# Kernel optimization log

Hardware: AMD Instinct MI355X
Metric: run time of the kernel (lower is better)

Reference implementation:

```python
import jax, jax.numpy as jnp
import numpy as np


def setup_inputs() -> dict:
    key = jax.random.key(0)
    ks = jax.random.split(key, 6)
    B, H, W, C = 4, 56, 56, 256
    NH, K = 8, 7
    return {
        "x": jax.random.normal(ks[0], (B, H, W, C), dtype=jnp.float32),
        "w_qkv": jax.random.normal(ks[1], (C, 3 * C), dtype=jnp.float32) * 0.02,
        "b_qkv": jax.random.normal(ks[2], (3 * C,), dtype=jnp.float32) * 0.02,
        "rpb": jax.random.normal(ks[3], (NH, K * K), dtype=jnp.float32) * 0.02,
        "w_proj": jax.random.normal(ks[4], (C, C), dtype=jnp.float32) * 0.02,
        "b_proj": jax.random.normal(ks[5], (C,), dtype=jnp.float32) * 0.02,
    }


def _window_stack(xp, H, W, ks):
    # xp: (B, H+2p, W+2p, nh, hd) zero-padded map.
    # Returns (B, H, W, nh, ks*ks, hd): each pixel's ks x ks neighborhood,
    # row-major (h offset outer, w offset inner) to match torch unfold order.
    return jnp.stack(
        [xp[:, i:i + H, j:j + W] for i in range(ks) for j in range(ks)],
        axis=-2,
    )


def reference(x, w_qkv, b_qkv, rpb, w_proj, b_proj):
    B, H, W, C = x.shape
    nh, ks2 = rpb.shape
    ks = int(np.sqrt(ks2) + 0.5)  # 7
    hd = C // nh
    scale = hd ** -0.5
    pad = ks // 2  # dilation == 1

    qkv = (x @ w_qkv + b_qkv).reshape(B, H, W, 3, nh, hd)
    q = qkv[..., 0, :, :] * scale        # (B,H,W,nh,hd)
    k = qkv[..., 1, :, :]
    v = qkv[..., 2, :, :]

    pads = ((0, 0), (pad, pad), (pad, pad), (0, 0), (0, 0))
    kw = _window_stack(jnp.pad(k, pads), H, W, ks)  # (B,H,W,nh,ks2,hd)
    vw = _window_stack(jnp.pad(v, pads), H, W, ks)

    # scores over each pixel's ks*ks neighbors (zero-padded borders kept,
    # matching the torch reference), plus relative position bias.
    attn = jnp.einsum("bhwnd,bhwnkd->bhwnk", q, kw) + rpb[None, None, None]
    attn = jax.nn.softmax(attn, axis=-1)
    out = jnp.einsum("bhwnk,bhwnkd->bhwnd", attn, vw).reshape(B, H, W, C)
    return out @ w_proj + b_proj
```

## Files before the change

kernel.cpp:

```cpp
#include <hip/hip_runtime.h>
#include <hip/hip_bf16.h>


using frag_ab = __attribute__((ext_vector_type(8))) short;
using f32x4   = __attribute__((ext_vector_type(4))) float;
using f32x2   = __attribute__((ext_vector_type(2))) float;

typedef const __attribute__((address_space(1))) unsigned int* gas_u32;
typedef __attribute__((address_space(3))) unsigned int*       las_u32;

__device__ __forceinline__ void gl_lds16(const void* g, void* l) {
    __builtin_amdgcn_global_load_lds((gas_u32)g, (las_u32)l, 16, 0, 0);
}

__device__ __forceinline__ float bflo(unsigned int u) { return __uint_as_float(u << 16); }
__device__ __forceinline__ float bfhi(unsigned int u) { return __uint_as_float(u & 0xffff0000u); }

__device__ __forceinline__ f32x2 unpk2(unsigned int u) {
    f32x2 r; r.x = bflo(u); r.y = bfhi(u); return r;
}

#if defined(__has_builtin)
#if __has_builtin(__builtin_amdgcn_fdot2_f32_bf16)
#define HAVE_FDOT2_BF16 1
#endif
#endif

#ifdef HAVE_FDOT2_BF16
typedef __bf16 bf16x2 __attribute__((ext_vector_type(2)));
__device__ __forceinline__ float dot2bf(unsigned int a, unsigned int b, float c) {
    union { unsigned int u; bf16x2 h; } ua, ub;
    ua.u = a; ub.u = b;
    return __builtin_amdgcn_fdot2_f32_bf16(ua.h, ub.h, c, false);
}
#endif

__global__ __launch_bounds__(256) void prep_k(
    const float* __restrict__ w_qkv,  __hip_bfloat16* __restrict__ wqkvT,
    const float* __restrict__ w_proj, __hip_bfloat16* __restrict__ wprojT,
    __hip_bfloat16* __restrict__ kp,  __hip_bfloat16* __restrict__ vp)
{
    const int bid = blockIdx.x;
    const int tid = threadIdx.x;
    if (bid < 768) {
        const int idx = bid * 256 + tid;
        const int k = idx & 255, n = idx >> 8;
        wqkvT[idx] = __float2bfloat16(w_qkv[k * 768 + n]);
    } else if (bid < 1024) {
        const int idx = (bid - 768) * 256 + tid;
        const int k = idx & 255, n = idx >> 8;
        wprojT[idx] = __float2bfloat16(w_proj[k * 256 + n]);
    } else {
        const int u    = (bid - 1024) * 256 + tid;
        const int ip   = u / 30720;
        const int rem  = u - ip * 30720;
        const int cloc = rem >> 5;
        const int q16  = rem & 31;
        const int img  = ip >> 1;
        __hip_bfloat16* base = (ip & 1) ? vp : kp;
        int prow, pcol;
        if (cloc < 512) {
            const int r8 = cloc >> 6;
            prow = (r8 < 3) ? r8 : r8 + 56;
            pcol = cloc & 63;
        } else {
            const int c2 = cloc - 512;
            prow = 3 + (c2 >> 3);
            const int cc = c2 & 7;
            pcol = (cc < 3) ? cc : cc + 56;
        }
        *(uint4*)(base + (((size_t)(img * 64 + prow)) * 64 + pcol) * 256 + q16 * 8) =
            make_uint4(0u, 0u, 0u, 0u);
    }
}

__global__ __launch_bounds__(256) void gemm_qkv_k(
    const float* __restrict__ X,
    const __hip_bfloat16* __restrict__ BT,
    const float* __restrict__ bias,
    __hip_bfloat16* __restrict__ qf,
    __hip_bfloat16* __restrict__ kp,
    __hip_bfloat16* __restrict__ vp,
    float qscale)
{
    constexpr int K = 256;
    __shared__ float   Asf[8][2][64][4];
    __shared__ frag_ab Bs[8][64];

    const int tid  = threadIdx.x;
    const int lane = tid & 63;
    const int w    = tid >> 6;
    const int wm   = w >> 1, wn = w & 1;
    const int m0 = blockIdx.y * 128;
    const int n0 = blockIdx.x * 128;

    const int lrow = lane & 15;
    const int lk   = (lane >> 4) * 8;
    const float* gA0 = X + (size_t)(m0 + (2*w+0)*16 + lrow) * K + lk;
    const float* gA1 = X + (size_t)(m0 + (2*w+1)*16 + lrow) * K + lk;
    const __hip_bfloat16* gB0 = BT + (size_t)(n0 + (2*w+0)*16 + lrow) * K + lk;
    const __hip_bfloat16* gB1 = BT + (size_t)(n0 + (2*w+1)*16 + lrow) * K + lk;

    f32x4 acc[4][4] = {};

    for (int k0 = 0; k0 < K; k0 += 32) {
        gl_lds16(gA0 + k0,     &Asf[2*w+0][0][0][0]);
        gl_lds16(gA0 + k0 + 4, &Asf[2*w+0][1][0][0]);
        gl_lds16(gA1 + k0,     &Asf[2*w+1][0][0][0]);
        gl_lds16(gA1 + k0 + 4, &Asf[2*w+1][1][0][0]);
        gl_lds16(gB0 + k0, &Bs[2*w+0][0]);
        gl_lds16(gB1 + k0, &Bs[2*w+1][0]);
        __syncthreads();
        frag_ab af[4], bf[4];
        #pragma unroll
        for (int i = 0; i < 4; ++i) {
            const float4 c0 = *(const float4*)&Asf[wm*4+i][0][lane][0];
            const float4 c1 = *(const float4*)&Asf[wm*4+i][1][lane][0];
            union { frag_ab f; __hip_bfloat16 h[8]; } u;
            u.h[0] = __float2bfloat16(c0.x); u.h[1] = __float2bfloat16(c0.y);
            u.h[2] = __float2bfloat16(c0.z); u.h[3] = __float2bfloat16(c0.w);
            u.h[4] = __float2bfloat16(c1.x); u.h[5] = __float2bfloat16(c1.y);
            u.h[6] = __float2bfloat16(c1.z); u.h[7] = __float2bfloat16(c1.w);
            af[i] = u.f;
            bf[i] = Bs[wn*4+i][lane];
        }
        #pragma unroll
        for (int i = 0; i < 4; ++i)
            #pragma unroll
            for (int j = 0; j < 4; ++j)
                acc[i][j] = __builtin_amdgcn_mfma_f32_16x16x32_bf16(af[i], bf[j], acc[i][j], 0, 0, 0);
        __syncthreads();
    }

    const int rbase = (lane >> 4) * 4;
    const int cbase = lane & 15;
    #pragma unroll
    for (int fi = 0; fi < 4; ++fi) {
        const int rm = m0 + wm * 64 + fi * 16 + rbase;
        #pragma unroll
        for (int fj = 0; fj < 4; ++fj) {
            const int cn = n0 + wn * 64 + fj * 16 + cbase;
            const float bv = bias[cn];
            #pragma unroll
            for (int r = 0; r < 4; ++r) {
                const int mm  = rm + r;
                const float val = acc[fi][fj][r] + bv;
                const int sel = cn >> 8;
                if (sel == 0) {
                    qf[(size_t)mm * 256 + cn] = __float2bfloat16(val * qscale);
                } else {
                    const int c  = cn & 255;
                    const int bb = mm / 3136;
                    const int r2 = mm % 3136;
                    const int yy = r2 / 56;
                    const int xx = r2 % 56;
                    __hip_bfloat16* dst = (sel == 1) ? kp : vp;
                    dst[(((size_t)(bb * 64 + yy + 3)) * 64 + (xx + 3)) * 256 + c] =
                        __float2bfloat16(val);
                }
            }
        }
    }
}

__global__ __launch_bounds__(256) void gemm_proj_k(
    const __hip_bfloat16* __restrict__ A,
    const __hip_bfloat16* __restrict__ BT,
    const float* __restrict__ bias,
    float* __restrict__ C)
{
    constexpr int K = 256;
    __shared__ frag_ab As[4][64];
    __shared__ frag_ab Bs[4][64];

    const int tid  = threadIdx.x;
    const int lane = tid & 63;
    const int w    = tid >> 6;
    const int wm   = w >> 1, wn = w & 1;
    const int m0 = blockIdx.y * 64;
    const int n0 = blockIdx.x * 64;

    const int lrow = lane & 15;
    const int lk   = (lane >> 4) * 8;
    const __hip_bfloat16* gA = A  + (size_t)(m0 + w * 16 + lrow) * K + lk;
    const __hip_bfloat16* gB = BT + (size_t)(n0 + w * 16 + lrow) * K + lk;

    f32x4 acc[2][2] = {};

    for (int k0 = 0; k0 < K; k0 += 32) {
        gl_lds16(gA + k0, &As[w][0]);
        gl_lds16(gB + k0, &Bs[w][0]);
        __syncthreads();
        const frag_ab a0 = As[2 * wm + 0][lane];
        const frag_ab a1 = As[2 * wm + 1][lane];
        const frag_ab b0 = Bs[2 * wn + 0][lane];
        const frag_ab b1 = Bs[2 * wn + 1][lane];
        acc[0][0] = __builtin_amdgcn_mfma_f32_16x16x32_bf16(a0, b0, acc[0][0], 0, 0, 0);
        acc[0][1] = __builtin_amdgcn_mfma_f32_16x16x32_bf16(a0, b1, acc[0][1], 0, 0, 0);
        acc[1][0] = __builtin_amdgcn_mfma_f32_16x16x32_bf16(a1, b0, acc[1][0], 0, 0, 0);
        acc[1][1] = __builtin_amdgcn_mfma_f32_16x16x32_bf16(a1, b1, acc[1][1], 0, 0, 0);
        __syncthreads();
    }

    const int rbase = (lane >> 4) * 4;
    const int cbase = lane & 15;
    #pragma unroll
    for (int fi = 0; fi < 2; ++fi) {
        const int rm = m0 + wm * 32 + fi * 16 + rbase;
        #pragma unroll
        for (int fj = 0; fj < 2; ++fj) {
            const int cn = n0 + wn * 32 + fj * 16 + cbase;
            const float bv = bias[cn];
            #pragma unroll
            for (int r = 0; r < 4; ++r)
                C[(size_t)(rm + r) * 256 + cn] = acc[fi][fj][r] + bv;
        }
    }
}

__global__ __launch_bounds__(64) void na2d_attn_k(
    const __hip_bfloat16* __restrict__ qf,
    const __hip_bfloat16* __restrict__ kp,
    const __hip_bfloat16* __restrict__ vp,
    const float* __restrict__ rpb,
    __hip_bfloat16* __restrict__ out)
{
    const int lane = threadIdx.x;
    const int q8   = lane & 3;
    const int h    = (lane >> 2) & 7;
    const int tl   = (lane >> 5) & 1;

    const int bid = blockIdx.x;
    const int seg = (bid & 7) * 784 + (bid >> 3);
    const int row = seg / 28;
    const int x0  = (seg % 28) * 2;
    const int b   = row / 56;
    const int y   = row % 56;
    const int t   = row * 56 + x0 + tl;
    const int prow0 = b * 64 + y;

    __shared__ __hip_bfloat16 kbuf[8 * 256];
    __shared__ float srpb[8 * 49];

    for (int i = lane; i < 8 * 49; i += 64) srpb[i] = rpb[i];
    __syncthreads();

    unsigned int qpk[4];
    {
        const uint4 qa = *(const uint4*)(qf + (size_t)t * 256 + h * 32 + q8 * 8);
        qpk[0] = qa.x; qpk[1] = qa.y; qpk[2] = qa.z; qpk[3] = qa.w;
    }
#ifndef HAVE_FDOT2_BF16
    f32x2 q2[4];
    #pragma unroll
    for (int i = 0; i < 4; ++i) q2[i] = unpk2(qpk[i]);
#endif

    const int wroff = lane * 16;
    const int rdoff = tl * 512 + h * 64 + q8 * 16;

#define GLOAD4(plane, ky, d0, d1, d2, d3)                                       \
    do {                                                                        \
        const char* rb_ = (const char*)((plane) +                               \
            ((size_t)(prow0 + (ky)) * 64 + x0) * 256 + lane * 8);               \
        d0 = *(const uint4*)(rb_);                                              \
        d1 = *(const uint4*)(rb_ + 1024);                                       \
        d2 = *(const uint4*)(rb_ + 2048);                                       \
        d3 = *(const uint4*)(rb_ + 3072);                                       \
    } while (0)

#define LWRITE4(buf, s0, s1, s2, s3)                                            \
    do {                                                                        \
        char* wb_ = (char*)(buf) + wroff;                                       \
        *(uint4*)(wb_)        = s0;                                             \
        *(uint4*)(wb_ + 1024) = s1;                                             \
        *(uint4*)(wb_ + 2048) = s2;                                             \
        *(uint4*)(wb_ + 3072) = s3;                                             \
    } while (0)

    const float* rp = &srpb[h * 49];
    float m = -1e30f, l = 0.f;
    f32x2 o2[4] = {};

    uint4 k0, k1, k2, k3;
    GLOAD4(kp, 0, k0, k1, k2, k3);

    #pragma unroll 1
    for (int ky = 0; ky < 7; ++ky) {
        LWRITE4(kbuf, k0, k1, k2, k3);
        const __hip_bfloat16* vrow = vp +
            ((size_t)(prow0 + ky) * 64 + x0 + tl) * 256 + h * 32 + q8 * 8;
        uint4 va[7];
        #pragma unroll
        for (int kx = 0; kx < 7; ++kx)
            va[kx] = *(const uint4*)(vrow + kx * 256);
        if (ky < 6) GLOAD4(kp, ky + 1, k0, k1, k2, k3);
        float lg[7];
        #pragma unroll
        for (int kx = 0; kx < 7; ++kx) {
            const uint4 w0 = *(const uint4*)((const char*)kbuf + rdoff + kx * 512);
#ifdef HAVE_FDOT2_BF16
            float s = 0.f;
            s = dot2bf(qpk[0], w0.x, s);
            s = dot2bf(qpk[1], w0.y, s);
            s = dot2bf(qpk[2], w0.z, s);
            s = dot2bf(qpk[3], w0.w, s);
#else
            f32x2 s2 = {0.f, 0.f};
            s2 += q2[0] * unpk2(w0.x);
            s2 += q2[1] * unpk2(w0.y);
            s2 += q2[2] * unpk2(w0.z);
            s2 += q2[3] * unpk2(w0.w);
            const float s = s2.x + s2.y;
#endif
            lg[kx] = s;
        }
        #pragma unroll
        for (int kx = 0; kx < 7; ++kx) {
            lg[kx] += __shfl_xor(lg[kx], 1, 64);
            lg[kx] += __shfl_xor(lg[kx], 2, 64);
            lg[kx] += rp[ky * 7 + kx];
        }
        float rmax = lg[0];
        #pragma unroll
        for (int kx = 1; kx < 7; ++kx) rmax = fmaxf(rmax, lg[kx]);
        const float mnew  = fmaxf(m, rmax);
        const float alpha = __expf(m - mnew);
        m = mnew;
        l *= alpha;
        const f32x2 alpha2 = {alpha, alpha};
        #pragma unroll
        for (int i = 0; i < 4; ++i) o2[i] *= alpha2;
        #pragma unroll
        for (int kx = 0; kx < 7; ++kx) {
            const float pr = __expf(lg[kx] - mnew);
            l += pr;
            const f32x2 pr2 = {pr, pr};
            const uint4 w0 = va[kx];
            o2[0] += pr2 * unpk2(w0.x);
            o2[1] += pr2 * unpk2(w0.y);
            o2[2] += pr2 * unpk2(w0.z);
            o2[3] += pr2 * unpk2(w0.w);
        }
    }
#undef GLOAD4
#undef LWRITE4

    const float inv = 1.f / l;
    union { uint4 u; __hip_bfloat16 hh[8]; } ob;
    #pragma unroll
    for (int i = 0; i < 4; ++i) {
        ob.hh[2 * i + 0] = __float2bfloat16(o2[i].x * inv);
        ob.hh[2 * i + 1] = __float2bfloat16(o2[i].y * inv);
    }
    *(uint4*)(out + (size_t)t * 256 + h * 32 + q8 * 8) = ob.u;
}

extern "C" void kernel_launch(void* const* d_in, const int* in_sizes, int n_in,
                              void* d_out, int out_size, void* d_ws, size_t ws_size,
                              hipStream_t stream)
{
    const float* x      = (const float*)d_in[0];
    const float* w_qkv  = (const float*)d_in[1];
    const float* b_qkv  = (const float*)d_in[2];
    const float* rpb    = (const float*)d_in[3];
    const float* w_proj = (const float*)d_in[4];
    const float* b_proj = (const float*)d_in[5];
    float* out = (float*)d_out;

    const int M = 12544;

    char* wsp = (char*)d_ws;
    __hip_bfloat16* qf    = (__hip_bfloat16*)wsp; wsp += (size_t)M * 256 * 2;
    __hip_bfloat16* kp    = (__hip_bfloat16*)wsp; wsp += (size_t)4 * 64 * 64 * 256 * 2;
    __hip_bfloat16* vp    = (__hip_bfloat16*)wsp; wsp += (size_t)4 * 64 * 64 * 256 * 2;
    __hip_bfloat16* attnb = (__hip_bfloat16*)wsp; wsp += (size_t)M * 256 * 2;
    __hip_bfloat16* wqkvT = (__hip_bfloat16*)wsp; wsp += (size_t)768 * 256 * 2;
    __hip_bfloat16* wprojT= (__hip_bfloat16*)wsp; wsp += (size_t)256 * 256 * 2;

    const float scale = 0.17677669529663689f;

    prep_k<<<1984, 256, 0, stream>>>(w_qkv, wqkvT, w_proj, wprojT, kp, vp);

    gemm_qkv_k<<<dim3(6, 98), 256, 0, stream>>>(x, wqkvT, b_qkv, qf, kp, vp, scale);

    na2d_attn_k<<<6272, 64, 0, stream>>>(qf, kp, vp, rpb, attnb);

    gemm_proj_k<<<dim3(4, 196), 256, 0, stream>>>(attnb, wprojT, b_proj, out);
}
```

Measured before the change: 137.9 us.

## Pre-convert x to bf16 and double-buffer LDS tiles in both GEMMs

The prep kernel gains a pass that converts the fp32 input x to a bf16 workspace copy. The QKV GEMM can then stage bf16 A tiles directly, with no fp32 LDS staging and no per-iteration conversion. Both the QKV and projection GEMMs now use two LDS buffers, so the next K-slice is fetched while the current one feeds the MFMAs. The cost is an extra global read and write of x in the prep kernel, plus doubled LDS footprint per block.

```diff
diff --git a/kernel.cpp b/kernel.cpp
--- a/kernel.cpp
+++ b/kernel.cpp
@@ -36,22 +36,30 @@
 #endif
 
 __global__ __launch_bounds__(256) void prep_k(
+    const float* __restrict__ x,      __hip_bfloat16* __restrict__ xb,
     const float* __restrict__ w_qkv,  __hip_bfloat16* __restrict__ wqkvT,
     const float* __restrict__ w_proj, __hip_bfloat16* __restrict__ wprojT,
     __hip_bfloat16* __restrict__ kp,  __hip_bfloat16* __restrict__ vp)
 {
     const int bid = blockIdx.x;
     const int tid = threadIdx.x;
-    if (bid < 768) {
-        const int idx = bid * 256 + tid;
+    if (bid < 3136) {
+        const int i = bid * 256 + tid;
+        const float4 v = ((const float4*)x)[i];
+        union { ushort4 u; __hip_bfloat16 h[4]; } o;
+        o.h[0] = __float2bfloat16(v.x); o.h[1] = __float2bfloat16(v.y);
+        o.h[2] = __float2bfloat16(v.z); o.h[3] = __float2bfloat16(v.w);
+        ((ushort4*)xb)[i] = o.u;
+    } else if (bid < 3904) {
+        const int idx = (bid - 3136) * 256 + tid;
         const int k = idx & 255, n = idx >> 8;
         wqkvT[idx] = __float2bfloat16(w_qkv[k * 768 + n]);
-    } else if (bid < 1024) {
-        const int idx = (bid - 768) * 256 + tid;
+    } else if (bid < 4160) {
+        const int idx = (bid - 3904) * 256 + tid;
         const int k = idx & 255, n = idx >> 8;
         wprojT[idx] = __float2bfloat16(w_proj[k * 256 + n]);
     } else {
-        const int u    = (bid - 1024) * 256 + tid;
+        const int u    = (bid - 4160) * 256 + tid;
         const int ip   = u / 30720;
         const int rem  = u - ip * 30720;
         const int cloc = rem >> 5;
@@ -75,7 +83,7 @@
 }
 
 __global__ __launch_bounds__(256) void gemm_qkv_k(
-    const float* __restrict__ X,
+    const __hip_bfloat16* __restrict__ A,
     const __hip_bfloat16* __restrict__ BT,
     const float* __restrict__ bias,
     __hip_bfloat16* __restrict__ qf,
@@ -84,8 +92,8 @@
     float qscale)
 {
     constexpr int K = 256;
-    __shared__ float   Asf[8][2][64][4];
-    __shared__ frag_ab Bs[8][64];
+    __shared__ frag_ab As[2][8][64];
+    __shared__ frag_ab Bs[2][8][64];
 
     const int tid  = threadIdx.x;
     const int lane = tid & 63;
@@ -96,33 +104,35 @@
 
     const int lrow = lane & 15;
     const int lk   = (lane >> 4) * 8;
-    const float* gA0 = X + (size_t)(m0 + (2*w+0)*16 + lrow) * K + lk;
-    const float* gA1 = X + (size_t)(m0 + (2*w+1)*16 + lrow) * K + lk;
+    const __hip_bfloat16* gA0 = A  + (size_t)(m0 + (2*w+0)*16 + lrow) * K + lk;
+    const __hip_bfloat16* gA1 = A  + (size_t)(m0 + (2*w+1)*16 + lrow) * K + lk;
     const __hip_bfloat16* gB0 = BT + (size_t)(n0 + (2*w+0)*16 + lrow) * K + lk;
     const __hip_bfloat16* gB1 = BT + (size_t)(n0 + (2*w+1)*16 + lrow) * K + lk;
 
     f32x4 acc[4][4] = {};
 
-    for (int k0 = 0; k0 < K; k0 += 32) {
-        gl_lds16(gA0 + k0,     &Asf[2*w+0][0][0][0]);
-        gl_lds16(gA0 + k0 + 4, &Asf[2*w+0][1][0][0]);
-        gl_lds16(gA1 + k0,     &Asf[2*w+1][0][0][0]);
-        gl_lds16(gA1 + k0 + 4, &Asf[2*w+1][1][0][0]);
-        gl_lds16(gB0 + k0, &Bs[2*w+0][0]);
-        gl_lds16(gB1 + k0, &Bs[2*w+1][0]);
-        __syncthreads();
+    gl_lds16(gA0, &As[0][2*w+0][0]);
+    gl_lds16(gA1, &As[0][2*w+1][0]);
+    gl_lds16(gB0, &Bs[0][2*w+0][0]);
+    gl_lds16(gB1, &Bs[0][2*w+1][0]);
+    __syncthreads();
+
+    #pragma unroll 1
+    for (int t = 0; t < 8; ++t) {
+        const int cur = t & 1;
+        if (t < 7) {
+            const int k0 = (t + 1) * 32;
+            const int nxt = cur ^ 1;
+            gl_lds16(gA0 + k0, &As[nxt][2*w+0][0]);
+            gl_lds16(gA1 + k0, &As[nxt][2*w+1][0]);
+            gl_lds16(gB0 + k0, &Bs[nxt][2*w+0][0]);
+            gl_lds16(gB1 + k0, &Bs[nxt][2*w+1][0]);
+        }
         frag_ab af[4], bf[4];
         #pragma unroll
         for (int i = 0; i < 4; ++i) {
-            const float4 c0 = *(const float4*)&Asf[wm*4+i][0][lane][0];
-            const float4 c1 = *(const float4*)&Asf[wm*4+i][1][lane][0];
-            union { frag_ab f; __hip_bfloat16 h[8]; } u;
-            u.h[0] = __float2bfloat16(c0.x); u.h[1] = __float2bfloat16(c0.y);
-            u.h[2] = __float2bfloat16(c0.z); u.h[3] = __float2bfloat16(c0.w);
-            u.h[4] = __float2bfloat16(c1.x); u.h[5] = __float2bfloat16(c1.y);
-            u.h[6] = __float2bfloat16(c1.z); u.h[7] = __float2bfloat16(c1.w);
-            af[i] = u.f;
-            bf[i] = Bs[wn*4+i][lane];
+            af[i] = As[cur][wm*4+i][lane];
+            bf[i] = Bs[cur][wn*4+i][lane];
         }
         #pragma unroll
         for (int i = 0; i < 4; ++i)
@@ -170,8 +180,8 @@
     float* __restrict__ C)
 {
     constexpr int K = 256;
-    __shared__ frag_ab As[4][64];
-    __shared__ frag_ab Bs[4][64];
+    __shared__ frag_ab As[2][4][64];
+    __shared__ frag_ab Bs[2][4][64];
 
     const int tid  = threadIdx.x;
     const int lane = tid & 63;
@@ -187,14 +197,23 @@
 
     f32x4 acc[2][2] = {};
 
-    for (int k0 = 0; k0 < K; k0 += 32) {
-        gl_lds16(gA + k0, &As[w][0]);
-        gl_lds16(gB + k0, &Bs[w][0]);
-        __syncthreads();
-        const frag_ab a0 = As[2 * wm + 0][lane];
-        const frag_ab a1 = As[2 * wm + 1][lane];
-        const frag_ab b0 = Bs[2 * wn + 0][lane];
-        const frag_ab b1 = Bs[2 * wn + 1][lane];
+    gl_lds16(gA, &As[0][w][0]);
+    gl_lds16(gB, &Bs[0][w][0]);
+    __syncthreads();
+
+    #pragma unroll 1
+    for (int t = 0; t < 8; ++t) {
+        const int cur = t & 1;
+        if (t < 7) {
+            const int k0 = (t + 1) * 32;
+            const int nxt = cur ^ 1;
+            gl_lds16(gA + k0, &As[nxt][w][0]);
+            gl_lds16(gB + k0, &Bs[nxt][w][0]);
+        }
+        const frag_ab a0 = As[cur][2 * wm + 0][lane];
+        const frag_ab a1 = As[cur][2 * wm + 1][lane];
+        const frag_ab b0 = Bs[cur][2 * wn + 0][lane];
+        const frag_ab b1 = Bs[cur][2 * wn + 1][lane];
         acc[0][0] = __builtin_amdgcn_mfma_f32_16x16x32_bf16(a0, b0, acc[0][0], 0, 0, 0);
         acc[0][1] = __builtin_amdgcn_mfma_f32_16x16x32_bf16(a0, b1, acc[0][1], 0, 0, 0);
         acc[1][0] = __builtin_amdgcn_mfma_f32_16x16x32_bf16(a1, b0, acc[1][0], 0, 0, 0);
@@ -374,15 +393,16 @@
     __hip_bfloat16* qf    = (__hip_bfloat16*)wsp; wsp += (size_t)M * 256 * 2;
     __hip_bfloat16* kp    = (__hip_bfloat16*)wsp; wsp += (size_t)4 * 64 * 64 * 256 * 2;
     __hip_bfloat16* vp    = (__hip_bfloat16*)wsp; wsp += (size_t)4 * 64 * 64 * 256 * 2;
+    __hip_bfloat16* xb    = (__hip_bfloat16*)wsp; wsp += (size_t)M * 256 * 2;
     __hip_bfloat16* attnb = (__hip_bfloat16*)wsp; wsp += (size_t)M * 256 * 2;
     __hip_bfloat16* wqkvT = (__hip_bfloat16*)wsp; wsp += (size_t)768 * 256 * 2;
     __hip_bfloat16* wprojT= (__hip_bfloat16*)wsp; wsp += (size_t)256 * 256 * 2;
 
     const float scale = 0.17677669529663689f;
 
-    prep_k<<<1984, 256, 0, stream>>>(w_qkv, wqkvT, w_proj, wprojT, kp, vp);
-
-    gemm_qkv_k<<<dim3(6, 98), 256, 0, stream>>>(x, wqkvT, b_qkv, qf, kp, vp, scale);
+    prep_k<<<5120, 256, 0, stream>>>(x, xb, w_qkv, wqkvT, w_proj, wprojT, kp, vp);
+
+    gemm_qkv_k<<<dim3(6, 98), 256, 0, stream>>>(xb, wqkvT, b_qkv, qf, kp, vp, scale);
 
     na2d_attn_k<<<6272, 64, 0, stream>>>(qf, kp, vp, rpb, attnb);
 
```

New measurement: 135.4 us. Within noise of the previous version (-1.8%).
